# Optimization experiments

Measured on AMD Instinct MI355X. Metric: run time of the kernel, lower is better.

Reference implementation:

```python
import jax, jax.numpy as jnp
import numpy as np

B, C, H, W = 4, 96, 256, 256
HEADS = 4
WH = WW = 8            # window size
QKV_D = C // HEADS     # qkv_dim defaults to in_channels // num_heads
N = WH * WW            # tokens per window
EPS = 1e-6


def _rel_index():
    # Swin-style relative position index, [N, N], constant
    coords = np.stack(np.meshgrid(np.arange(WH), np.arange(WW), indexing='ij'), 0).reshape(2, -1)
    rel = coords[:, :, None] - coords[:, None, :]
    rel[0] += WH - 1
    rel[1] += WW - 1
    return rel[0] * (2 * WW - 1) + rel[1]

REL = jnp.asarray(_rel_index())  # int32 [N, N]


def setup_inputs() -> dict:
    key = jax.random.key(0)
    ks = jax.random.split(key, 8)
    s = lambda k, shape: jax.random.normal(k, shape, jnp.float32) * 0.02
    return dict(
        x=jax.random.normal(ks[0], (B, C, H, W), jnp.float32),
        norm_w=jnp.ones((C,), jnp.float32),                      # RMSNorm inside MHA (channel-last tokens)
        qkv_w=s(ks[1], (3 * HEADS * QKV_D, C)),
        qkv_b=jnp.zeros((3 * HEADS * QKV_D,), jnp.float32),
        proj_w=s(ks[2], (C, HEADS * QKV_D)),
        proj_b=jnp.zeros((C,), jnp.float32),
        bias_table=s(ks[3], ((2 * WH - 1) * (2 * WW - 1),)),     # WindowScoreBias table (shared across heads)
        mlp_norm_w=jnp.ones((1, C, 1, 1), jnp.float32),          # RMSNorm1((1,C,1,1), dim=1)
        w1_w=s(ks[4], (2 * C, C, 1, 1)),                         # mid = out_channels*mlp_ratio = 2C
        w1_b=jnp.zeros((2 * C,), jnp.float32),
        w2_w=s(ks[5], (C, C, 3, 3)),                             # mid//2 = C -> C, 3x3
        w2_b=jnp.zeros((C,), jnp.float32),
    )


def rms_norm(x, w, axis):
    v = jnp.mean(x * x, axis=axis, keepdims=True)
    return x * jax.lax.rsqrt(v + EPS) * w


def conv2d(x, w, b):
    y = jax.lax.conv_general_dilated(x, w, (1, 1), 'VALID',
                                     dimension_numbers=('NCHW', 'OIHW', 'NCHW'))
    return y + b[None, :, None, None]


def reference(x, norm_w, qkv_w, qkv_b, proj_w, proj_b, bias_table,
              mlp_norm_w, w1_w, w1_b, w2_w, w2_b):
    B_, C_, H_, W_ = x.shape
    nH, nW = H_ // WH, W_ // WW
    # ---- windowed MHA with norm fused in and relative bias ----
    # window partition: [B,C,H,W] -> [B*nWin, N, C]
    xw = x.reshape(B_, C_, nH, WH, nW, WW).transpose(0, 2, 4, 3, 5, 1).reshape(-1, N, C_)
    xn = rms_norm(xw, norm_w, -1)
    qkv = xn @ qkv_w.T + qkv_b                                  # [Bn, N, 3*h*d]
    qkv = qkv.reshape(-1, N, 3, HEADS, QKV_D).transpose(2, 0, 3, 1, 4)  # [3, Bn, h, N, d]
    q, k, v = qkv[0], qkv[1], qkv[2]
    bias = bias_table[REL]                                      # [N, N], broadcast over batch/heads
    scores = jnp.einsum('bhnd,bhmd->bhnm', q, k) / jnp.sqrt(jnp.float32(QKV_D)) + bias
    attn = jax.nn.softmax(scores, axis=-1)
    o = jnp.einsum('bhnm,bhmd->bhnd', attn, v)
    o = o.transpose(0, 2, 1, 3).reshape(-1, N, HEADS * QKV_D)
    o = o @ proj_w.T + proj_b
    # reverse window partition
    o = o.reshape(B_, nH, nW, WH, WW, C_).transpose(0, 5, 1, 3, 2, 4).reshape(B_, C_, H_, W_)
    x = x + o
    # ---- GLU conv MLP residual ----
    y = rms_norm(x, mlp_norm_w, 1)
    y = conv2d(y, w1_w, w1_b)                                   # 1x1, C -> 2C
    a, g = jnp.split(y, 2, axis=1)
    y = a * jax.nn.sigmoid(g)                                   # GLU along channels
    # ReplicationPad2dDetach: edge pad whose padded ring carries no gradient
    yp = jnp.pad(jax.lax.stop_gradient(y), ((0, 0), (0, 0), (1, 1), (1, 1)), mode='edge')
    yp = yp.at[:, :, 1:-1, 1:-1].set(y)
    y = conv2d(yp, w2_w, w2_b)                                  # 3x3 valid on padded -> same size
    y = jnp.where(y >= 0, y, 0.1 * y)                           # leaky_relu(0.1)
    return x + y
```

## Files before the change

### kernel.cpp

```cpp
#include <hip/hip_runtime.h>
#include <hip/hip_bf16.h>

#define CC 96

typedef short short8  __attribute__((ext_vector_type(8)));
typedef short short4v __attribute__((ext_vector_type(4)));
typedef float f32x4   __attribute__((ext_vector_type(4)));
typedef _Float16 half4 __attribute__((ext_vector_type(4)));

#if __has_builtin(__builtin_amdgcn_mfma_f32_16x16x16_f16)
  #define MFMA16(a,b,c) __builtin_amdgcn_mfma_f32_16x16x16_f16((a),(b),(c),0,0,0)
#else
  #define MFMA16(a,b,c) __builtin_amdgcn_mfma_f32_16x16x16f16((a),(b),(c),0,0,0)
#endif

static __device__ __forceinline__ ushort f2bf(float f) {
  __hip_bfloat16 h = __float2bfloat16(f);
  return *reinterpret_cast<ushort*>(&h);
}
static __device__ __forceinline__ float bf2f(ushort u) {
  union { unsigned int u; float f; } v; v.u = ((unsigned int)u) << 16; return v.f;
}

#define QSCALE 0.20412414523193154f

__global__ void prep_kernel(const float* __restrict__ qkv_w,
                            const float* __restrict__ qkv_b,
                            const float* __restrict__ proj_w,
                            const float* __restrict__ w2w,
                            const float* __restrict__ w1w,
                            __hip_bfloat16* __restrict__ qkvp,
                            float* __restrict__ qkvb2,
                            __hip_bfloat16* __restrict__ projp,
                            __hip_bfloat16* __restrict__ w2p,
                            __hip_bfloat16* __restrict__ w1p,
                            __hip_bfloat16* __restrict__ vwp)
{
  const int i = blockIdx.x*256 + threadIdx.x;
  if (i < 36864) {
    const int e = i & 7, lane = (i >> 3) & 63;
    const int rest = i >> 9;
    const int mt = rest % 6, r2 = rest / 6;
    const int ks = r2 % 3, h = r2 / 3;
    const int od = mt*16 + (lane & 15);
    const int sec = od >> 5, d = od & 31;
    const int c = ks*32 + (lane >> 4)*8 + e;
    float val = 0.f;
    if (d < 24) {
      val = qkv_w[(sec*96 + h*24 + d)*96 + c];
      if (sec == 0) val *= QSCALE;
    }
    qkvp[i] = __float2bfloat16(val);
  }
  const int jb = i - 36864;
  if (jb >= 0 && jb < 384) {
    const int h = jb / 96, od = jb - h*96;
    const int sec = od >> 5, d = od & 31;
    float val = 0.f;
    if (d < 24) {
      val = qkv_b[sec*96 + h*24 + d];
      if (sec == 0) val *= QSCALE;
    }
    qkvb2[jb] = val;
  }
  const int j = i - 37248;
  if (j >= 0 && j < 9216) {
    const int e = j & 7, lane = (j >> 3) & 63;
    const int rest = j >> 9;
    const int nt = rest % 6, ks = rest / 6;
    const int oc = nt*16 + (lane & 15);
    const int dd = ks*32 + (lane >> 4)*8 + e;
    projp[j] = __float2bfloat16(proj_w[oc*96 + dd]);
  }
  const int k = i - 46464;
  if (k >= 0 && k < 82944) {
    const int e = k & 7;
    const int lane = (k >> 3) & 63;
    const int rest = k >> 9;
    const int nf = rest % 6;
    const int r2 = rest / 6;
    const int kc = r2 % 3;
    const int tap = r2 / 3;
    const int cidx = kc*32 + (lane >> 4)*8 + e;
    const int oc = nf*16 + (lane & 15);
    const int ky = tap / 3, kx = tap - ky*3;
    w2p[k] = __float2bfloat16(w2w[((oc*96 + cidx)*3 + ky)*3 + kx]);
  }
  const int m = i - 129408;
  if (m >= 0 && m < 18432) {
    const int e = m & 7, lane = (m >> 3) & 63;
    const int rest = m >> 9;
    const int nt = rest % 12, ks = rest / 12;
    const int oc = nt*16 + (lane & 15);
    const int c  = ks*32 + (lane >> 4)*8 + e;
    w1p[m] = __float2bfloat16(w1w[oc*96 + c]);
  }
  const int v = i - 147840;
  if (v >= 0 && v < 12288) {
    const int e = v & 7, lane = (v >> 3) & 63;
    const int rest = v >> 9;
    const int nt2 = rest % 2, r2 = rest / 2;
    const int ks = r2 % 3, h = r2 / 3;
    const int d = nt2*16 + (lane & 15);
    const int c = ks*32 + (lane >> 4)*8 + e;
    const float val = (d < 24) ? qkv_w[(192 + h*24 + d)*96 + c] : 0.f;
    vwp[v] = __float2bfloat16(val);
  }
}

__global__ __launch_bounds__(512, 2) void attn_kernel(
    const float* __restrict__ x,
    const float* __restrict__ norm_w,
    const __hip_bfloat16* __restrict__ qkvp,
    const float* __restrict__ qkvb2,
    const __hip_bfloat16* __restrict__ vwp,
    const __hip_bfloat16* __restrict__ projp,
    const float* __restrict__ proj_b,
    const float* __restrict__ bias_table,
    float* __restrict__ out)
{
  extern __shared__ char smem[];
  ushort* xn   = (ushort*)smem;
  ushort* xr   = (ushort*)(smem + 26624);
  float*  btab = (float*)(smem + 51200);

  const int wp = blockIdx.x;
  const int b   = wp >> 9;
  const int wy  = (wp >> 4) & 31;
  const int wxp = wp & 15;
  const int t  = threadIdx.x;
  const int y0 = wy*8, x0 = wxp*16;
  const int l  = t & 63;
  const int W  = __builtin_amdgcn_readfirstlane(t >> 6);
  const int w2 = W >> 2, h = W & 3;
  const int lr = l & 15, g = l >> 4;

  for (int i = t; i < 225; i += 512) btab[i] = bias_table[i];

  {
    const int p = t >> 2, q = t & 3;
    const int ty = p >> 4, tx = p & 15;
    const float* xp = x + (size_t)(b*CC + q*24)*65536 + (size_t)(y0+ty)*256 + x0 + tx;
    float xv[24]; float ss = 0.f;
    #pragma unroll
    for (int i = 0; i < 24; i++) { xv[i] = xp[(size_t)i*65536]; ss += xv[i]*xv[i]; }
    ss += __shfl_xor(ss, 1);
    ss += __shfl_xor(ss, 2);
    const float s = rsqrtf(ss * (1.f/96.f) + 1e-6f);
    const int row = (tx >> 3)*64 + ty*8 + (tx & 7);
    #pragma unroll
    for (int k2 = 0; k2 < 3; k2++) {
      short8 pk, pr;
      #pragma unroll
      for (int q2 = 0; q2 < 8; q2++) {
        pr[q2] = (short)f2bf(xv[k2*8+q2]);
        pk[q2] = (short)f2bf(xv[k2*8+q2] * s * norm_w[q*24 + k2*8 + q2]);
      }
      *(short8*)(xn + row*104 + q*24 + k2*8) = pk;
      *(short8*)(xr + row*96  + q*24 + k2*8) = pr;
    }
  }
  __syncthreads();

  half4 qf[2][4], kf[2][4];
  #pragma unroll
  for (int pass = 0; pass < 2; pass++) {
    f32x4 acc[2][4];
    #pragma unroll
    for (int m2 = 0; m2 < 2; m2++)
      #pragma unroll
      for (int nt = 0; nt < 4; nt++) acc[m2][nt] = (f32x4)0.f;
    #pragma unroll
    for (int ks = 0; ks < 3; ks++) {
      short8 bfr[4];
      #pragma unroll
      for (int nt = 0; nt < 4; nt++)
        bfr[nt] = *(const short8*)((const char*)xn + (w2*64 + nt*16 + lr)*208 + g*16 + ks*64);
      #pragma unroll
      for (int m2 = 0; m2 < 2; m2++) {
        const short8 afr = *(const short8*)(qkvp + ((h*3+ks)*6 + pass*2 + m2)*512 + l*8);
        #pragma unroll
        for (int nt = 0; nt < 4; nt++)
          acc[m2][nt] = __builtin_amdgcn_mfma_f32_16x16x32_bf16(afr, bfr[nt], acc[m2][nt], 0, 0, 0);
      }
    }
    #pragma unroll
    for (int m2 = 0; m2 < 2; m2++) {
      const f32x4 bb = *(const f32x4*)(qkvb2 + h*96 + (pass*2+m2)*16 + g*4);
      #pragma unroll
      for (int nt = 0; nt < 4; nt++)
        #pragma unroll
        for (int r = 0; r < 4; r++) {
          const float v = acc[m2][nt][r] + bb[r];
          if (pass == 0) qf[m2][nt][r] = (_Float16)v;
          else           kf[m2][nt][r] = (_Float16)v;
        }
    }
  }

  half4 pa[4][4];
  #pragma unroll
  for (int qt = 0; qt < 4; qt++) {
    f32x4 sacc[4];
    #pragma unroll
    for (int kt = 0; kt < 4; kt++) {
      f32x4 s0 = MFMA16(kf[0][kt], qf[0][qt], (f32x4)0.f);
      sacc[kt] = MFMA16(kf[1][kt], qf[1][qt], s0);
    }
    const int q = qt*16 + lr;
    const int aq = (q >> 3)*15 + (q & 7);
    float vv[4][4];
    float mx = -1e30f;
    #pragma unroll
    for (int kt = 0; kt < 4; kt++)
      #pragma unroll
      for (int r = 0; r < 4; r++) {
        const int k = kt*16 + g*4 + r;
        vv[kt][r] = sacc[kt][r] + btab[aq + 112 - ((k >> 3)*15 + (k & 7))];
        mx = fmaxf(mx, vv[kt][r]);
      }
    mx = fmaxf(mx, __shfl_xor(mx, 16));
    mx = fmaxf(mx, __shfl_xor(mx, 32));
    float sum = 0.f;
    #pragma unroll
    for (int kt = 0; kt < 4; kt++)
      #pragma unroll
      for (int r = 0; r < 4; r++) { vv[kt][r] = __expf(vv[kt][r] - mx); sum += vv[kt][r]; }
    sum += __shfl_xor(sum, 16);
    sum += __shfl_xor(sum, 32);
    const float rinv = 1.f / sum;
    #pragma unroll
    for (int kt = 0; kt < 4; kt++)
      #pragma unroll
      for (int r = 0; r < 4; r++) pa[kt][qt][r] = (_Float16)(vv[kt][r] * rinv);
  }

  half4 vb[4][2];
  {
    f32x4 vacc[4][2];
    #pragma unroll
    for (int kt = 0; kt < 4; kt++) { vacc[kt][0] = (f32x4)0.f; vacc[kt][1] = (f32x4)0.f; }
    #pragma unroll
    for (int ks = 0; ks < 3; ks++) {
      short8 afr[4];
      #pragma unroll
      for (int kt = 0; kt < 4; kt++)
        afr[kt] = *(const short8*)((const char*)xn + (w2*64 + kt*16 + lr)*208 + g*16 + ks*64);
      #pragma unroll
      for (int nt2 = 0; nt2 < 2; nt2++) {
        const short8 vwf = *(const short8*)(vwp + ((h*3+ks)*2+nt2)*512 + l*8);
        #pragma unroll
        for (int kt = 0; kt < 4; kt++)
          vacc[kt][nt2] = __builtin_amdgcn_mfma_f32_16x16x32_bf16(afr[kt], vwf, vacc[kt][nt2], 0, 0, 0);
      }
    }
    #pragma unroll
    for (int nt2 = 0; nt2 < 2; nt2++) {
      const float vbias = qkvb2[h*96 + 64 + nt2*16 + lr];
      #pragma unroll
      for (int kt = 0; kt < 4; kt++)
        #pragma unroll
        for (int r = 0; r < 4; r++)
          vb[kt][nt2][r] = (_Float16)(vacc[kt][nt2][r] + vbias);
    }
  }

  f32x4 oacc[4][2];
  #pragma unroll
  for (int qt = 0; qt < 4; qt++) { oacc[qt][0] = (f32x4)0.f; oacc[qt][1] = (f32x4)0.f; }
  #pragma unroll
  for (int kt = 0; kt < 4; kt++)
    #pragma unroll
    for (int qt = 0; qt < 4; qt++) {
      oacc[qt][0] = MFMA16(pa[kt][qt], vb[kt][0], oacc[qt][0]);
      oacc[qt][1] = MFMA16(pa[kt][qt], vb[kt][1], oacc[qt][1]);
    }
  __syncthreads();

  #pragma unroll
  for (int qt = 0; qt < 4; qt++)
    #pragma unroll
    for (int r = 0; r < 4; r++) {
      const int row = w2*64 + qt*16 + g*4 + r;
      xn[row*104 + h*24 + lr] = f2bf(oacc[qt][0][r]);
      if (lr < 8) xn[row*104 + h*24 + 16 + lr] = f2bf(oacc[qt][1][r]);
    }
  __syncthreads();

  {
    f32x4 pacc[6];
    #pragma unroll
    for (int nt = 0; nt < 6; nt++) pacc[nt] = (f32x4)0.f;
    #pragma unroll
    for (int ks = 0; ks < 3; ks++) {
      const short8 af = *(const short8*)((const char*)xn + (lr + W*16)*208 + g*16 + ks*64);
      #pragma unroll
      for (int nt = 0; nt < 6; nt++) {
        const short8 bf = *(const short8*)(projp + (ks*6+nt)*512 + l*8);
        pacc[nt] = __builtin_amdgcn_mfma_f32_16x16x32_bf16(af, bf, pacc[nt], 0, 0, 0);
      }
    }
    __syncthreads();
    ushort* oT = xn;
    #pragma unroll
    for (int nt = 0; nt < 6; nt++) {
      const int oc = lr + nt*16;
      const float bias = proj_b[oc];
      short4v pk;
      #pragma unroll
      for (int r = 0; r < 4; r++) {
        const int row = W*16 + g*4 + r;
        pk[r] = (short)f2bf(pacc[nt][r] + bias + bf2f(xr[row*96 + oc]));
      }
      *(short4v*)((char*)oT + oc*264 + (g*4 + W*16)*2) = pk;
    }
  }
  __syncthreads();

  {
    const ushort* oT = xn;
    #pragma unroll
    for (int k2 = 0; k2 < 6; k2++) {
      const int e = t + k2*512;
      const int oc = e >> 5, q5 = e & 31;
      const int ty = q5 >> 2, tq = q5 & 3;
      const int m = (tq >> 1)*64 + ty*8 + (tq & 1)*4;
      const short4v ov = *(const short4v*)((const char*)oT + oc*264 + m*2);
      const size_t gidx = (size_t)(b*CC+oc)*65536 + (size_t)(y0+ty)*256 + x0 + tq*4;
      float4 res;
      res.x = bf2f((ushort)ov[0]);
      res.y = bf2f((ushort)ov[1]);
      res.z = bf2f((ushort)ov[2]);
      res.w = bf2f((ushort)ov[3]);
      *(float4*)(out + gidx) = res;
    }
  }
}

__global__ __launch_bounds__(256, 2) void mlp1_kernel(
    const float* __restrict__ x1,
    const float* __restrict__ mlp_norm_w,
    const __hip_bfloat16* __restrict__ w1p,
    const float* __restrict__ w1_b,
    __hip_bfloat16* __restrict__ y)
{
  __shared__ ushort xn[128*104];
  const int blk = blockIdx.x;
  const int b   = blk >> 9;
  const int p0  = (blk & 511) << 7;
  const int t   = threadIdx.x;
  const int l   = t & 63;
  const int w   = __builtin_amdgcn_readfirstlane(t >> 6);
  const int lr  = l & 15, g = l >> 4;

  {
    const int p = t >> 1, half = t & 1;
    const float* xp = x1 + (size_t)(b*CC + half*48)*65536 + p0 + p;
    float xv[48];
    float ss = 0.f;
    #pragma unroll
    for (int i = 0; i < 48; i++) { xv[i] = xp[(size_t)i*65536]; ss += xv[i]*xv[i]; }
    ss += __shfl_xor(ss, 1);
    const float s = rsqrtf(ss*(1.f/96.f) + 1e-6f);
    #pragma unroll
    for (int i = 0; i < 48; i += 2) {
      const int c = half*48 + i;
      union { ushort u[2]; uint v; } pk;
      pk.u[0] = f2bf(xv[i]   * s * mlp_norm_w[c]);
      pk.u[1] = f2bf(xv[i+1] * s * mlp_norm_w[c+1]);
      *(uint*)(&xn[p*104 + c]) = pk.v;
    }
  }

  f32x4 acc[2][12];
  #pragma unroll
  for (int m2 = 0; m2 < 2; m2++)
    #pragma unroll
    for (int nt = 0; nt < 12; nt++) acc[m2][nt] = (f32x4)0.f;

  #pragma unroll
  for (int ks = 0; ks < 3; ks++) {
    short8 afr[2];
    #pragma unroll
    for (int m2 = 0; m2 < 2; m2++)
      afr[m2] = *(const short8*)((const char*)xn + (lr + (w*2+m2)*16)*208 + g*16 + ks*64);
    #pragma unroll
    for (int nt = 0; nt < 12; nt++) {
      const short8 bfr = *(const short8*)(w1p + ((ks*12+nt)*64 + l)*8);
      #pragma unroll
      for (int m2 = 0; m2 < 2; m2++)
        acc[m2][nt] = __builtin_amdgcn_mfma_f32_16x16x32_bf16(afr[m2], bfr, acc[m2][nt], 0, 0, 0);
    }
  }

  #pragma unroll
  for (int m2 = 0; m2 < 2; m2++)
    #pragma unroll
    for (int nt = 0; nt < 6; nt++) {
      const int oc = nt*16 + lr;
      const float ab = w1_b[oc], gb = w1_b[96+oc];
      #pragma unroll
      for (int r = 0; r < 4; r++) {
        const int row = (w*2+m2)*16 + g*4 + r;
        const float a  = acc[m2][nt][r]   + ab;
        const float gg = acc[m2][nt+6][r] + gb;
        xn[row*104 + oc] = f2bf(a / (1.f + __expf(-gg)));
      }
    }
  __syncthreads();

  __hip_bfloat16* yp = y + ((size_t)(b*65536 + p0))*96;
  #pragma unroll
  for (int k2 = 0; k2 < 6; k2++) {
    const int e = t + k2*256;
    const int p = e / 12, ch = e - p*12;
    const short8 v = *(const short8*)(&xn[p*104 + ch*8]);
    *(short8*)((ushort*)yp + p*96 + ch*8) = v;
  }
}

__global__ __launch_bounds__(256, 2) void conv3_kernel(
    const __hip_bfloat16* __restrict__ y,
    const __hip_bfloat16* __restrict__ w2p,
    const float* __restrict__ w2_b,
    float* __restrict__ xout)
{
  extern __shared__ char smem[];
  ushort* A  = (ushort*)smem;
  ushort* Bs = (ushort*)(smem + 54912);

  const int vbid = (blockIdx.x & 7)*256 + (blockIdx.x >> 3);
  const int b   = vbid >> 9;
  const int rem = vbid & 511;
  const int ch  = rem >> 7;
  const int rp  = rem & 127;
  const int px0 = ch << 6;
  const int t   = threadIdx.x;
  const int w   = __builtin_amdgcn_readfirstlane(t >> 6);
  const int l   = t & 63;
  const int m15 = l & 15, lh = l >> 4;

  for (int e = t; e < 3168; e += 256) {
    const int seg  = e / 12;
    const int part = e - seg*12;
    const int ky = seg / 66;
    const int px = seg - ky*66;
    const int gy = min(255, max(0, 2*rp + ky - 1));
    const int gx = min(255, max(0, px0 + px - 1));
    const short8 v = *(const short8*)(y + ((size_t)(b*65536 + gy*256 + gx))*96 + part*8);
    *(short8*)(A + seg*104 + part*8) = v;
  }

  f32x4 resid[2][6];
  const int gpx = px0 + 16*w + lh*4;
  #pragma unroll
  for (int rw = 0; rw < 2; rw++)
    #pragma unroll
    for (int nf = 0; nf < 6; nf++) {
      const int oc = nf*16 + m15;
      resid[rw][nf] = *(const f32x4*)(xout + ((size_t)(b*CC + oc))*65536 + (size_t)(2*rp+rw)*256 + gpx);
    }

  uint2 breg[9];
  {
    const uint2* src = (const uint2*)w2p;
    #pragma unroll
    for (int i = 0; i < 9; i++) breg[i] = src[t + i*256];
  }

  f32x4 acc0[6], acc1[6];
  #pragma unroll
  for (int nf = 0; nf < 6; ++nf) { acc0[nf] = (f32x4)0.f; acc1[nf] = (f32x4)0.f; }

  for (int tap = 0; tap < 9; ++tap) {
    __syncthreads();
    {
      uint2* dst = (uint2*)Bs;
      #pragma unroll
      for (int i = 0; i < 9; i++) dst[t + i*256] = breg[i];
    }
    if (tap < 8) {
      const uint2* src = (const uint2*)w2p + (tap+1)*2304;
      #pragma unroll
      for (int i = 0; i < 9; i++) breg[i] = src[t + i*256];
    }
    __syncthreads();

    const int ky = tap / 3, kx = tap - ky*3;
    #pragma unroll
    for (int kc = 0; kc < 3; ++kc) {
      const int cb = kc*32 + lh*8;
      const short8 a0 = *(const short8*)(A + ((ky  )*66 + 16*w + m15 + kx)*104 + cb);
      const short8 a1 = *(const short8*)(A + ((ky+1)*66 + 16*w + m15 + kx)*104 + cb);
      #pragma unroll
      for (int nf = 0; nf < 6; ++nf) {
        const short8 bf = *(const short8*)(Bs + ((kc*6+nf)*64 + l)*8);
        acc0[nf] = __builtin_amdgcn_mfma_f32_16x16x32_bf16(a0, bf, acc0[nf], 0, 0, 0);
        acc1[nf] = __builtin_amdgcn_mfma_f32_16x16x32_bf16(a1, bf, acc1[nf], 0, 0, 0);
      }
    }
  }

  #pragma unroll
  for (int nf = 0; nf < 6; ++nf) {
    const int oc = nf*16 + m15;
    const float bb = w2_b[oc];
    #pragma unroll
    for (int rw = 0; rw < 2; rw++) {
      const f32x4 av = rw ? acc1[nf] : acc0[nf];
      float* op = xout + ((size_t)(b*CC + oc))*65536 + (size_t)(2*rp+rw)*256 + gpx;
      f32x4 r = resid[rw][nf];
      #pragma unroll
      for (int q = 0; q < 4; ++q) {
        float u = av[q] + bb;
        u = (u >= 0.f) ? u : 0.1f*u;
        r[q] += u;
      }
      *(f32x4*)op = r;
    }
  }
}

extern "C" void kernel_launch(void* const* d_in, const int* in_sizes, int n_in,
                              void* d_out, int out_size, void* d_ws, size_t ws_size,
                              hipStream_t stream)
{
  (void)in_sizes; (void)n_in; (void)out_size; (void)ws_size;
  const float* x      = (const float*)d_in[0];
  const float* norm_w = (const float*)d_in[1];
  const float* qkv_w  = (const float*)d_in[2];
  const float* qkv_b  = (const float*)d_in[3];
  const float* proj_w = (const float*)d_in[4];
  const float* proj_b = (const float*)d_in[5];
  const float* btab   = (const float*)d_in[6];
  const float* mlpnw  = (const float*)d_in[7];
  const float* w1w    = (const float*)d_in[8];
  const float* w1b    = (const float*)d_in[9];
  const float* w2w    = (const float*)d_in[10];
  const float* w2b    = (const float*)d_in[11];
  float* out = (float*)d_out;

  char* ws = (char*)d_ws;
  __hip_bfloat16* y     = (__hip_bfloat16*)ws;
  __hip_bfloat16* w2p   = (__hip_bfloat16*)(ws + 50331648);
  __hip_bfloat16* qkvp  = (__hip_bfloat16*)(ws + 50497536);
  float*          qkvb2 = (float*)(ws + 50571264);
  __hip_bfloat16* projp = (__hip_bfloat16*)(ws + 50572800);
  __hip_bfloat16* w1p   = (__hip_bfloat16*)(ws + 50591232);
  __hip_bfloat16* vwp   = (__hip_bfloat16*)(ws + 50628096);

  prep_kernel<<<626, 256, 0, stream>>>(qkv_w, qkv_b, proj_w, w2w, w1w,
                                       qkvp, qkvb2, projp, w2p, w1p, vwp);

  attn_kernel<<<2048, 512, 52100, stream>>>(x, norm_w, qkvp, qkvb2, vwp, projp, proj_b, btab, out);
  mlp1_kernel<<<2048, 256, 0, stream>>>(out, mlpnw, w1p, w1b, y);
  conv3_kernel<<<2048, 256, 73344, stream>>>(y, w2p, w2b, out);
}
```

Measured before the change: 232.5 us.

## Store attention residual as window-blocked bf16 intermediate instead of fp32 output

The attention kernel now writes its residual output as bf16 into a workspace buffer laid out by window and channel. The MLP and conv kernels read this compact buffer instead of the fp32 output tensor. The MLP kernel also switches its pixel mapping to follow window tiles. The aim is to halve the bytes of the intermediate written and read twice. The cost is that the residual is held in bf16 rather than fp32, and the new path only runs if the workspace is large enough, otherwise the old fp32 path is kept.

```diff
diff --git a/kernel.cpp b/kernel.cpp
--- a/kernel.cpp
+++ b/kernel.cpp
@@ -117,7 +117,8 @@
     const __hip_bfloat16* __restrict__ projp,
     const float* __restrict__ proj_b,
     const float* __restrict__ bias_table,
-    float* __restrict__ out)
+    float* __restrict__ out,
+    ushort* __restrict__ x1b)
 {
   extern __shared__ char smem[];
   ushort* xn   = (ushort*)smem;
@@ -126,6 +127,7 @@
 
   const int wp = blockIdx.x;
   const int b   = wp >> 9;
+  const int wpl = wp & 511;
   const int wy  = (wp >> 4) & 31;
   const int wxp = wp & 15;
   const int t  = threadIdx.x;
@@ -317,7 +319,18 @@
   }
   __syncthreads();
 
-  {
+  if (x1b) {
+    const ushort* oT = xn;
+    #pragma unroll
+    for (int k2 = 0; k2 < 6; k2++) {
+      const int e = t + k2*512;
+      const int oc = e >> 5, q5 = e & 31;
+      const int ty = q5 >> 2, tq = q5 & 3;
+      const int m = (tq >> 1)*64 + ty*8 + (tq & 1)*4;
+      const short4v ov = *(const short4v*)((const char*)oT + oc*264 + m*2);
+      *(short4v*)(x1b + ((size_t)(b*96+oc)*512 + wpl)*128 + m) = ov;
+    }
+  } else {
     const ushort* oT = xn;
     #pragma unroll
     for (int k2 = 0; k2 < 6; k2++) {
@@ -338,7 +351,8 @@
 }
 
 __global__ __launch_bounds__(256, 2) void mlp1_kernel(
-    const float* __restrict__ x1,
+    const float* __restrict__ x1f,
+    const ushort* __restrict__ x1b,
     const float* __restrict__ mlp_norm_w,
     const __hip_bfloat16* __restrict__ w1p,
     const float* __restrict__ w1_b,
@@ -347,7 +361,8 @@
   __shared__ ushort xn[128*104];
   const int blk = blockIdx.x;
   const int b   = blk >> 9;
-  const int p0  = (blk & 511) << 7;
+  const int wpl = blk & 511;
+  const int wy  = wpl >> 4, wxp = wpl & 15;
   const int t   = threadIdx.x;
   const int l   = t & 63;
   const int w   = __builtin_amdgcn_readfirstlane(t >> 6);
@@ -355,11 +370,19 @@
 
   {
     const int p = t >> 1, half = t & 1;
-    const float* xp = x1 + (size_t)(b*CC + half*48)*65536 + p0 + p;
     float xv[48];
     float ss = 0.f;
-    #pragma unroll
-    for (int i = 0; i < 48; i++) { xv[i] = xp[(size_t)i*65536]; ss += xv[i]*xv[i]; }
+    if (x1b) {
+      const ushort* xp = x1b + ((size_t)(b*96 + half*48)*512 + wpl)*128 + p;
+      #pragma unroll
+      for (int i = 0; i < 48; i++) { xv[i] = bf2f(xp[(size_t)i*65536]); ss += xv[i]*xv[i]; }
+    } else {
+      const int gy = wy*8 + ((p & 63) >> 3);
+      const int gx = wxp*16 + (p >> 6)*8 + (p & 7);
+      const float* xp = x1f + (size_t)(b*CC + half*48)*65536 + (size_t)gy*256 + gx;
+      #pragma unroll
+      for (int i = 0; i < 48; i++) { xv[i] = xp[(size_t)i*65536]; ss += xv[i]*xv[i]; }
+    }
     ss += __shfl_xor(ss, 1);
     const float s = rsqrtf(ss*(1.f/96.f) + 1e-6f);
     #pragma unroll
@@ -409,13 +432,14 @@
     }
   __syncthreads();
 
-  __hip_bfloat16* yp = y + ((size_t)(b*65536 + p0))*96;
   #pragma unroll
   for (int k2 = 0; k2 < 6; k2++) {
     const int e = t + k2*256;
     const int p = e / 12, ch = e - p*12;
+    const int gy = wy*8 + ((p & 63) >> 3);
+    const int gx = wxp*16 + (p >> 6)*8 + (p & 7);
     const short8 v = *(const short8*)(&xn[p*104 + ch*8]);
-    *(short8*)((ushort*)yp + p*96 + ch*8) = v;
+    *(short8*)((ushort*)y + ((size_t)(b*65536 + gy*256 + gx))*96 + ch*8) = v;
   }
 }
 
@@ -423,6 +447,7 @@
     const __hip_bfloat16* __restrict__ y,
     const __hip_bfloat16* __restrict__ w2p,
     const float* __restrict__ w2_b,
+    const ushort* __restrict__ x1b,
     float* __restrict__ xout)
 {
   extern __shared__ char smem[];
@@ -453,13 +478,30 @@
 
   f32x4 resid[2][6];
   const int gpx = px0 + 16*w + lh*4;
-  #pragma unroll
-  for (int rw = 0; rw < 2; rw++)
-    #pragma unroll
-    for (int nf = 0; nf < 6; nf++) {
-      const int oc = nf*16 + m15;
-      resid[rw][nf] = *(const f32x4*)(xout + ((size_t)(b*CC + oc))*65536 + (size_t)(2*rp+rw)*256 + gpx);
-    }
+  if (x1b) {
+    #pragma unroll
+    for (int rw = 0; rw < 2; rw++) {
+      const int gyo = 2*rp + rw;
+      const int wpl = (gyo >> 3)*16 + (gpx >> 4);
+      const int gx4 = gpx & 15;
+      const int m = (gx4 >> 3)*64 + (gyo & 7)*8 + (gx4 & 7);
+      #pragma unroll
+      for (int nf = 0; nf < 6; nf++) {
+        const int oc = nf*16 + m15;
+        const short4v rv = *(const short4v*)(x1b + ((size_t)(b*96+oc)*512 + wpl)*128 + m);
+        #pragma unroll
+        for (int q = 0; q < 4; q++) resid[rw][nf][q] = bf2f((ushort)rv[q]);
+      }
+    }
+  } else {
+    #pragma unroll
+    for (int rw = 0; rw < 2; rw++)
+      #pragma unroll
+      for (int nf = 0; nf < 6; nf++) {
+        const int oc = nf*16 + m15;
+        resid[rw][nf] = *(const f32x4*)(xout + ((size_t)(b*CC + oc))*65536 + (size_t)(2*rp+rw)*256 + gpx);
+      }
+  }
 
   uint2 breg[9];
   {
@@ -525,7 +567,7 @@
                               void* d_out, int out_size, void* d_ws, size_t ws_size,
                               hipStream_t stream)
 {
-  (void)in_sizes; (void)n_in; (void)out_size; (void)ws_size;
+  (void)in_sizes; (void)n_in; (void)out_size;
   const float* x      = (const float*)d_in[0];
   const float* norm_w = (const float*)d_in[1];
   const float* qkv_w  = (const float*)d_in[2];
@@ -548,11 +590,15 @@
   __hip_bfloat16* projp = (__hip_bfloat16*)(ws + 50572800);
   __hip_bfloat16* w1p   = (__hip_bfloat16*)(ws + 50591232);
   __hip_bfloat16* vwp   = (__hip_bfloat16*)(ws + 50628096);
+  const size_t X1B_OFF = 50652672;
+  const size_t X1B_END = X1B_OFF + (size_t)4*96*512*128*2;
+  ushort* x1b = (ws_size >= X1B_END) ? (ushort*)(ws + X1B_OFF) : nullptr;
 
   prep_kernel<<<626, 256, 0, stream>>>(qkv_w, qkv_b, proj_w, w2w, w1w,
                                        qkvp, qkvb2, projp, w2p, w1p, vwp);
 
-  attn_kernel<<<2048, 512, 52100, stream>>>(x, norm_w, qkvp, qkvb2, vwp, projp, proj_b, btab, out);
-  mlp1_kernel<<<2048, 256, 0, stream>>>(out, mlpnw, w1p, w1b, y);
-  conv3_kernel<<<2048, 256, 73344, stream>>>(y, w2p, w2b, out);
+  attn_kernel<<<2048, 512, 52100, stream>>>(x, norm_w, qkvp, qkvb2, vwp, projp, proj_b, btab,
+                                            out, x1b);
+  mlp1_kernel<<<2048, 256, 0, stream>>>(out, x1b, mlpnw, w1p, w1b, y);
+  conv3_kernel<<<2048, 256, 73344, stream>>>(y, w2p, w2b, x1b, out);
 }
```

New measurement: 227.7 us. 2.1% less time.
